# Kernel optimization log

Hardware: AMD Instinct MI355X
Metric: run time of the kernel (lower is better)

Reference implementation:

```python
import jax, jax.numpy as jnp
import numpy as np

B, T, C, H, N = 4, 1024, 1024, 16, 64
DW, DA, DV, DG = 64, 64, 64, 160  # LoRA ranks derived from C=1024
LNX_EPS = 0.00064


def layer_norm(h, g, b, eps=1e-5):
    m = h.mean(-1, keepdims=True)
    var = ((h - m) ** 2).mean(-1, keepdims=True)
    return (h - m) * jax.lax.rsqrt(var + eps) * g + b


def token_shift(h):
    # nn.ZeroPad2d((0,0,1,-1)): shift right along T, zero at t=0
    return jnp.pad(h, ((0, 0), (1, 0), (0, 0)))[:, :-1]


def wkv7(r, w, k, v, a, b):
    # RWKV-7 generalized recurrence. Inputs [B,T,C]; w is log-space decay.
    def re(t):
        return t.reshape(B, T, H, N).transpose(1, 0, 2, 3)  # -> [T,B,H,N]
    r, w, k, v, a, b = map(re, (r, w, k, v, a, b))
    dec = jnp.exp(-jnp.exp(w))
    S0 = jnp.zeros((B, H, N, N), r.dtype)  # state: [value_dim, key_dim]
    def step(S, ins):
        r_, d_, k_, v_, a_, b_ = ins
        sa = jnp.einsum('bhij,bhj->bhi', S, a_)
        S = S * d_[:, :, None, :] + sa[..., None] * b_[:, :, None, :] + v_[..., None] * k_[:, :, None, :]
        return S, jnp.einsum('bhij,bhj->bhi', S, r_)
    _, out = jax.lax.scan(step, S0, (r, dec, k, v, a, b))
    return out.transpose(1, 0, 2, 3).reshape(B, T, C)


def _forward(x, v_first, ln1_g, ln1_b, ln2_g, ln2_b, x_r, x_w, x_k_mix, x_v_mix, x_a, x_g,
             w0, w1, w2, a0, a1, a2, v0, v1, v2, g1, g2, k_k, k_a, r_k,
             W_r, W_k, W_v, W_o, lnx_g, lnx_b, xk_c, Wk_ff, Wv_ff):
    # ---- RNW_Tmix (original RWKV-7 path, layer_id > 0) ----
    h = layer_norm(x, ln1_g, ln1_b)
    xx = token_shift(h) - h
    xr = h + xx * x_r
    xw = h + xx * x_w
    xk = h + xx * x_k_mix
    xv = h + xx * x_v_mix
    xa = h + xx * x_a
    xg = h + xx * x_g
    r = xr @ W_r.T
    w = -jax.nn.softplus(-(w0 + jnp.tanh(xw @ w1) @ w2)) - 0.5
    k = xk @ W_k.T
    v = xv @ W_v.T
    v = v + (v_first - v) * jax.nn.sigmoid(v0 + (xv @ v1) @ v2)
    a = jax.nn.sigmoid(a0 + (xa @ a1) @ a2)
    g = jax.nn.sigmoid(xg @ g1) @ g2
    kk = (k * k_k).reshape(B, T, H, N)
    kk = kk / jnp.maximum(jnp.linalg.norm(kk, axis=-1, keepdims=True), 1e-12)
    kk = kk.reshape(B, T, C)
    k = k * (1 + (a - 1) * k_a)
    y = wkv7(r, w, k, v, -kk, kk * a)
    # GroupNorm(H groups of N channels), eps=0.00064
    yg = y.reshape(B, T, H, N)
    m = yg.mean(-1, keepdims=True)
    var = ((yg - m) ** 2).mean(-1, keepdims=True)
    y = ((yg - m) * jax.lax.rsqrt(var + LNX_EPS)).reshape(B, T, C) * lnx_g + lnx_b
    r4 = r.reshape(B, T, H, N)
    k4 = k.reshape(B, T, H, N)
    v4 = v.reshape(B, T, H, N)
    y = y + ((r4 * k4 * r_k).sum(-1, keepdims=True) * v4).reshape(B, T, C)
    x = x + (y * g) @ W_o.T
    # ---- RWKV_CMix_x070 ----
    h2 = layer_norm(x, ln2_g, ln2_b)
    hx = token_shift(h2) - h2
    kf = h2 + hx * xk_c
    kf = jnp.square(jax.nn.relu(kf @ Wk_ff.T))
    x = x + kf @ Wv_ff.T
    return x


def setup_inputs() -> dict:
    key = jax.random.key(0)
    ks = jax.random.split(key, 40)
    it = iter(range(40))
    def rn(shape, s=0.02):
        return (jax.random.normal(ks[next(it)], shape) * s).astype(jnp.float32)
    def ru(shape):
        return jax.random.uniform(ks[next(it)], shape).astype(jnp.float32)
    return {
        'x': rn((B, T, C), 1.0),
        'v_first': rn((B, T, C), 1.0),
        'ln1_g': jnp.ones((C,), jnp.float32), 'ln1_b': jnp.zeros((C,), jnp.float32),
        'ln2_g': jnp.ones((C,), jnp.float32), 'ln2_b': jnp.zeros((C,), jnp.float32),
        'x_r': ru((1, 1, C)), 'x_w': ru((1, 1, C)), 'x_k_mix': ru((1, 1, C)),
        'x_v_mix': ru((1, 1, C)), 'x_a': ru((1, 1, C)), 'x_g': ru((1, 1, C)),
        'w0': rn((1, 1, C), 0.5) - 4.0, 'w1': rn((C, DW)), 'w2': rn((DW, C), 0.1),
        'a0': rn((1, 1, C), 0.3), 'a1': rn((C, DA)), 'a2': rn((DA, C), 0.1),
        'v0': rn((1, 1, C), 0.3) + 0.73, 'v1': rn((C, DV)), 'v2': rn((DV, C), 0.1),
        'g1': rn((C, DG)), 'g2': rn((DG, C), 0.1),
        'k_k': rn((1, 1, C), 0.05) + 0.71, 'k_a': rn((1, 1, C), 0.05) + 1.02,
        'r_k': rn((H, N), 0.05) - 0.04,
        'W_r': rn((C, C)), 'W_k': rn((C, C), 0.002), 'W_v': rn((C, C)), 'W_o': rn((C, C)),
        'lnx_g': jnp.ones((C,), jnp.float32), 'lnx_b': jnp.zeros((C,), jnp.float32),
        'xk_c': ru((1, 1, C)),
        'Wk_ff': rn((4 * C, C)), 'Wv_ff': rn((C, 4 * C)),
    }


def reference(x, v_first, ln1_g, ln1_b, ln2_g, ln2_b, x_r, x_w, x_k_mix, x_v_mix, x_a, x_g,
              w0, w1, w2, a0, a1, a2, v0, v1, v2, g1, g2, k_k, k_a, r_k,
              W_r, W_k, W_v, W_o, lnx_g, lnx_b, xk_c, Wk_ff, Wv_ff):
    return _forward(x, v_first, ln1_g, ln1_b, ln2_g, ln2_b, x_r, x_w, x_k_mix, x_v_mix, x_a, x_g,
                    w0, w1, w2, a0, a1, a2, v0, v1, v2, g1, g2, k_k, k_a, r_k,
                    W_r, W_k, W_v, W_o, lnx_g, lnx_b, xk_c, Wk_ff, Wv_ff)
```

## Files before the change

kernel.cpp:

```cpp
#include <hip/hip_runtime.h>
#include <hip/hip_bf16.h>


#define BB 4
#define TT 1024
#define CC 1024
#define HH 16
#define NHEAD 64
#define MTOK 4096
#define FFDIM 4096

using bf16 = __hip_bfloat16;
typedef __attribute__((ext_vector_type(8))) short short8;
typedef __attribute__((ext_vector_type(4))) float f32x4;

__device__ __forceinline__ float b2f(bf16 x) { return __bfloat162float(x); }
__device__ __forceinline__ bf16 f2b(float x) { return __float2bfloat16(x); }
__device__ __forceinline__ float u2f(unsigned short u) {
  return __uint_as_float((unsigned)u << 16);
}
__device__ __forceinline__ float4 cv4(ushort4 u) {
  return make_float4(u2f(u.x), u2f(u.y), u2f(u.z), u2f(u.w));
}
__device__ __forceinline__ float ldin(const void* p, size_t i, int m) {
  return m ? b2f(((const bf16*)p)[i]) : ((const float*)p)[i];
}

__device__ __forceinline__ void async16(const void* g, void* l) {
  __builtin_amdgcn_global_load_lds((const __attribute__((address_space(1))) void*)g,
                                   (__attribute__((address_space(3))) void*)l, 16, 0, 0);
}

__device__ __forceinline__ float rowsum16(float x) {
  int t;
  t = __builtin_amdgcn_update_dpp(0, __float_as_int(x), 0x121, 0xF, 0xF, true);
  x += __int_as_float(t);
  t = __builtin_amdgcn_update_dpp(0, __float_as_int(x), 0x122, 0xF, 0xF, true);
  x += __int_as_float(t);
  t = __builtin_amdgcn_update_dpp(0, __float_as_int(x), 0x124, 0xF, 0xF, true);
  x += __int_as_float(t);
  t = __builtin_amdgcn_update_dpp(0, __float_as_int(x), 0x128, 0xF, 0xF, true);
  x += __int_as_float(t);
  return x;
}

__global__ void probe_kernel(const unsigned int* g, int* flag) {
  if (threadIdx.x == 0 && blockIdx.x == 0) {
    flag[0] = (g[0] == 0x3F800000u) ? 0 : 1;
    flag[1] = 1;
  }
}

__global__ __launch_bounds__(256) void cvt_all(
    const void* wr, const void* wk, const void* wv, const void* wo,
    const void* wkff, const void* wvff, const int* flagp,
    bf16* wrc, bf16* wkc, bf16* wvc, bf16* woc, bf16* wkffc, bf16* wvffc) {
  const int z = blockIdx.z;
  const void* in; bf16* out; int n4;
  const int nCC4 = CC * CC / 4, nFF4 = FFDIM * CC / 4;
  switch (z) {
    case 0: in = wr;   out = wrc;   n4 = nCC4; break;
    case 1: in = wk;   out = wkc;   n4 = nCC4; break;
    case 2: in = wv;   out = wvc;   n4 = nCC4; break;
    case 3: in = wo;   out = woc;   n4 = nCC4; break;
    case 4: in = wkff; out = wkffc; n4 = nFF4; break;
    default: in = wvff; out = wvffc; n4 = nFF4; break;
  }
  const int fl = *flagp;
  const int i4 = blockIdx.x * 256 + threadIdx.x;
  if (i4 >= n4) return;
  const size_t i = (size_t)i4 * 4;
#pragma unroll
  for (int e = 0; e < 4; ++e) out[i + e] = f2b(ldin(in, i + e, fl));
}

__global__ __launch_bounds__(256) void fillmark_kernel(unsigned short* out, int n) {
  const int i = blockIdx.x * 256 + threadIdx.x;
  if (i < n) out[i] = 0x3F80;
}

template<int XM>
__global__ __launch_bounds__(256) void ln_kernel(const void* __restrict__ x,
    const void* __restrict__ g, const void* __restrict__ be, const int* flagp,
    bf16* __restrict__ out, float eps) {
  const int fl = *flagp;
  const int xm = (XM < 0) ? fl : XM;
  const int tid = threadIdx.x;
  const size_t base = (size_t)blockIdx.x * CC + tid * 4;
  float v[4];
#pragma unroll
  for (int e = 0; e < 4; ++e) v[e] = ldin(x, base + e, xm);
  float s  = v[0] + v[1] + v[2] + v[3];
  float ss = v[0]*v[0] + v[1]*v[1] + v[2]*v[2] + v[3]*v[3];
#pragma unroll
  for (int m = 1; m <= 32; m <<= 1) { s += __shfl_xor(s, m); ss += __shfl_xor(ss, m); }
  __shared__ float red[8];
  const int wave = tid >> 6, lane = tid & 63;
  if (lane == 0) { red[wave] = s; red[4 + wave] = ss; }
  __syncthreads();
  s  = red[0] + red[1] + red[2] + red[3];
  ss = red[4] + red[5] + red[6] + red[7];
  const float mean = s * (1.0f / CC);
  const float var  = ss * (1.0f / CC) - mean * mean;
  const float rstd = rsqrtf(var + eps);
#pragma unroll
  for (int e = 0; e < 4; ++e) {
    const int c = tid * 4 + e;
    out[base + e] = f2b((v[e] - mean) * rstd * ldin(g, c, fl) + ldin(be, c, fl));
  }
}

__global__ __launch_bounds__(256) void mix6_kernel(const bf16* __restrict__ h,
    const void* cr, const void* cw, const void* ck,
    const void* cv, const void* ca, const void* cg, const int* flagp,
    bf16* __restrict__ xr, bf16* __restrict__ xw, bf16* __restrict__ xk,
    bf16* __restrict__ xv, bf16* __restrict__ xa, bf16* __restrict__ xg) {
  const int fl = *flagp;
  const size_t idx = (size_t)blockIdx.x * 256 + threadIdx.x;
  const int c = idx & (CC - 1);
  const int t = (idx >> 10) & (TT - 1);
  const float hv = b2f(h[idx]);
  const float xx = (t == 0 ? 0.f : b2f(h[idx - CC])) - hv;
  xr[idx] = f2b(hv + xx * ldin(cr, c, fl));
  xw[idx] = f2b(hv + xx * ldin(cw, c, fl));
  xk[idx] = f2b(hv + xx * ldin(ck, c, fl));
  xv[idx] = f2b(hv + xx * ldin(cv, c, fl));
  xa[idx] = f2b(hv + xx * ldin(ca, c, fl));
  xg[idx] = f2b(hv + xx * ldin(cg, c, fl));
}

__global__ __launch_bounds__(256) void mix1_kernel(const bf16* __restrict__ h,
    const void* cf, const int* flagp, bf16* __restrict__ out) {
  const int fl = *flagp;
  const size_t idx = (size_t)blockIdx.x * 256 + threadIdx.x;
  const int c = idx & (CC - 1);
  const int t = (idx >> 10) & (TT - 1);
  const float hv = b2f(h[idx]);
  const float xx = (t == 0 ? 0.f : b2f(h[idx - CC])) - hv;
  out[idx] = f2b(hv + xx * ldin(cf, c, fl));
}

__global__ __launch_bounds__(256) void transpose_all(
    const void* w1, const void* a1, const void* v1, const void* g1,
    const void* w2, const void* a2, const void* v2, const void* g2,
    const int* flagp,
    bf16* w1t, bf16* a1t, bf16* v1t, bf16* g1t,
    bf16* w2t, bf16* a2t, bf16* v2t, bf16* g2t) {
  const int z = blockIdx.z;
  const void* in; bf16* out; int R, Cc;
  switch (z) {
    case 0: in = w1; out = w1t; R = CC;  Cc = 64;  break;
    case 1: in = a1; out = a1t; R = CC;  Cc = 64;  break;
    case 2: in = v1; out = v1t; R = CC;  Cc = 64;  break;
    case 3: in = g1; out = g1t; R = CC;  Cc = 160; break;
    case 4: in = w2; out = w2t; R = 64;  Cc = CC;  break;
    case 5: in = a2; out = a2t; R = 64;  Cc = CC;  break;
    case 6: in = v2; out = v2t; R = 64;  Cc = CC;  break;
    default: in = g2; out = g2t; R = 160; Cc = CC; break;
  }
  const int fl = *flagp;
  const int idx = blockIdx.x * 256 + threadIdx.x;
  if (idx >= R * Cc) return;
  const int r = idx / Cc, c = idx - r * Cc;
  out[(size_t)c * R + r] = f2b(ldin(in, idx, fl));
}

__device__ __forceinline__ void gemm_core(const bf16* __restrict__ A,
    const bf16* __restrict__ Bm, bf16* __restrict__ Out, int M, int N, int K,
    int mode, short* As, short* Bs) {
  const int tid  = threadIdx.x;
  const int wave = tid >> 6;
  const int lane = tid & 63;
  const int m0 = blockIdx.y * 128;
  const int n0 = blockIdx.x * 128;
  const int wr = (wave >> 1) * 64;
  const int wc = (wave & 1) * 64;
  const int lrow = lane & 15;
  const int lq   = lane >> 4;
  f32x4 acc[4][4];
#pragma unroll
  for (int i = 0; i < 4; ++i)
#pragma unroll
    for (int j = 0; j < 4; ++j) acc[i][j] = (f32x4){0.f, 0.f, 0.f, 0.f};

  for (int k0 = 0; k0 < K; k0 += 32) {
#pragma unroll
    for (int j = 0; j < 2; ++j) {
      const int chunk = j * 256 + tid;
      const int row = chunk >> 2;
      const int c8  = (chunk & 3) * 8;
      const int ldsbase = (j * 256 + wave * 64) * 8;
      const bf16* ga = A + (size_t)(m0 + row) * K + (k0 + c8);
      int br = n0 + row; br = br < N ? br : N - 1;
      const bf16* gb = Bm + (size_t)br * K + (k0 + c8);
      async16(ga, &As[ldsbase]);
      async16(gb, &Bs[ldsbase]);
    }
    __syncthreads();
    short8 af[4], bfr[4];
#pragma unroll
    for (int mi = 0; mi < 4; ++mi)
      af[mi] = *(const short8*)&As[(wr + mi * 16 + lrow) * 32 + lq * 8];
#pragma unroll
    for (int ni = 0; ni < 4; ++ni)
      bfr[ni] = *(const short8*)&Bs[(wc + ni * 16 + lrow) * 32 + lq * 8];
#pragma unroll
    for (int mi = 0; mi < 4; ++mi)
#pragma unroll
      for (int ni = 0; ni < 4; ++ni)
        acc[mi][ni] = __builtin_amdgcn_mfma_f32_16x16x32_bf16(af[mi], bfr[ni], acc[mi][ni], 0, 0, 0);
    __syncthreads();
  }
#pragma unroll
  for (int mi = 0; mi < 4; ++mi) {
#pragma unroll
    for (int ni = 0; ni < 4; ++ni) {
      const int col = n0 + wc + ni * 16 + lrow;
      if (col < N) {
#pragma unroll
        for (int rr = 0; rr < 4; ++rr) {
          const int rowg = m0 + wr + mi * 16 + lq * 4 + rr;
          const size_t oidx = (size_t)rowg * N + col;
          const float val = acc[mi][ni][rr];
          if (mode == 1) { const float t = val > 0.f ? val : 0.f; Out[oidx] = f2b(t * t); }
          else if (mode == 2) Out[oidx] = f2b(val);
          else if (mode == 3) Out[oidx] = f2b(tanhf(val));
          else Out[oidx] = f2b(1.f / (1.f + expf(-val)));
        }
      }
    }
  }
}

template<int MODE>
__global__ __launch_bounds__(256) void gemm_mf(const bf16* __restrict__ A,
    const bf16* __restrict__ Bm, bf16* __restrict__ Out, int M, int N, int K) {
  __shared__ short As[128 * 32];
  __shared__ short Bs[128 * 32];
  gemm_core(A, Bm, Out, M, N, K, MODE, As, Bs);
}

__global__ __launch_bounds__(256) void gemm_lora1(
    const bf16* xw, const bf16* xa, const bf16* xv, const bf16* xg,
    const bf16* w1t, const bf16* a1t, const bf16* v1t, const bf16* g1t,
    bf16* wm, bf16* am, bf16* vm, bf16* gm) {
  __shared__ short As[128 * 32];
  __shared__ short Bs[128 * 32];
  const int z = blockIdx.z;
  const bf16* A; const bf16* B; bf16* O; int N; int mode;
  if (z == 0)      { A = xw; B = w1t; O = wm; N = 64;  mode = 3; }
  else if (z == 1) { A = xa; B = a1t; O = am; N = 64;  mode = 2; }
  else if (z == 2) { A = xv; B = v1t; O = vm; N = 64;  mode = 2; }
  else             { A = xg; B = g1t; O = gm; N = 160; mode = 4; }
  if ((int)blockIdx.x * 128 >= N) return;
  gemm_core(A, B, O, MTOK, N, CC, mode, As, Bs);
}

__global__ __launch_bounds__(256) void gemm_lora2(
    const bf16* wm, const bf16* am, const bf16* vm, const bf16* gm,
    const bf16* w2t, const bf16* a2t, const bf16* v2t, const bf16* g2t,
    bf16* wl, bf16* al, bf16* vl, bf16* gb) {
  __shared__ short As[128 * 32];
  __shared__ short Bs[128 * 32];
  const int z = blockIdx.z;
  const bf16* A; const bf16* B; bf16* O; int K;
  if (z == 0)      { A = wm; B = w2t; O = wl; K = 64;  }
  else if (z == 1) { A = am; B = a2t; O = al; K = 64;  }
  else if (z == 2) { A = vm; B = v2t; O = vl; K = 64;  }
  else             { A = gm; B = g2t; O = gb; K = 160; }
  gemm_core(A, B, O, MTOK, CC, K, 2, As, Bs);
}

template<int MODE>
__global__ __launch_bounds__(256) void gemm_bt(const bf16* __restrict__ A,
    const void* __restrict__ Bm, const int* bmp, bf16* __restrict__ Out,
    int M, int N, int K) {
  const int bm = *bmp;
  __shared__ float As[64][17];
  __shared__ float Bs[64][17];
  const int tid = threadIdx.x;
  const int m0 = blockIdx.y * 64;
  const int n0 = blockIdx.x * 64;
  const int ty = tid >> 4, tx = tid & 15;
  float acc[4][4] = {};
  for (int k0 = 0; k0 < K; k0 += 16) {
    __syncthreads();
#pragma unroll
    for (int e = 0; e < 4; ++e) {
      const int lin = e * 256 + tid;
      const int row = lin >> 4;
      const int kk  = lin & 15;
      As[row][kk] = b2f(A[(size_t)(m0 + row) * K + k0 + kk]);
      int br = n0 + row; br = br < N ? br : N - 1;
      Bs[row][kk] = ldin(Bm, (size_t)br * K + k0 + kk, bm);
    }
    __syncthreads();
#pragma unroll
    for (int k = 0; k < 16; ++k) {
      float a[4], b[4];
#pragma unroll
      for (int i = 0; i < 4; ++i) a[i] = As[ty * 4 + i][k];
#pragma unroll
      for (int j = 0; j < 4; ++j) b[j] = Bs[tx * 4 + j][k];
#pragma unroll
      for (int i = 0; i < 4; ++i)
#pragma unroll
        for (int j = 0; j < 4; ++j) acc[i][j] += a[i] * b[j];
    }
  }
#pragma unroll
  for (int i = 0; i < 4; ++i) {
    const int rowg = m0 + ty * 4 + i;
#pragma unroll
    for (int j = 0; j < 4; ++j) {
      const int col = n0 + tx * 4 + j;
      if (col < N) {
        const size_t oidx = (size_t)rowg * N + col;
        const float val = acc[i][j];
        if (MODE == 1) { const float t = val > 0.f ? val : 0.f; Out[oidx] = f2b(t * t); }
        else if (MODE == 2) Out[oidx] = f2b(val);
        else if (MODE == 3) Out[oidx] = f2b(tanhf(val));
        else Out[oidx] = f2b(1.f / (1.f + expf(-val)));
      }
    }
  }
}

__global__ __launch_bounds__(256) void combine_kernel(
    bf16* kf, bf16* vf, bf16* wl, bf16* al, bf16* vl,
    const void* vfirst, const void* w0, const void* a0, const void* v0,
    const void* kkp, const void* kap, const int* flagp, float* decp) {
  const int fl = *flagp;
  const int tid = threadIdx.x;
  const size_t base = (size_t)blockIdx.x * CC + tid * 4;
  float kkv[4], av4[4];
  float ssq = 0.f;
#pragma unroll
  for (int e = 0; e < 4; ++e) {
    const int c = tid * 4 + e;
    const size_t idx = base + e;
    const float u = ldin(w0, c, fl) + b2f(wl[idx]);
    const float w = (u > 0.f ? -log1pf(expf(-u)) : u - log1pf(expf(u))) - 0.5f;
    wl[idx] = f2b(w);
    if (decp) decp[idx] = __expf(-__expf(w));
    const float a  = 1.f / (1.f + expf(-(ldin(a0, c, fl) + b2f(al[idx]))));
    const float vg = 1.f / (1.f + expf(-(ldin(v0, c, fl) + b2f(vl[idx]))));
    const float v = b2f(vf[idx]);
    vf[idx] = f2b(v + (ldin(vfirst, idx, fl) - v) * vg);
    const float kv = b2f(kf[idx]);
    const float kkr = kv * ldin(kkp, c, fl);
    kkv[e] = kkr; av4[e] = a;
    ssq += kkr * kkr;
    kf[idx] = f2b(kv * (1.f + (a - 1.f) * ldin(kap, c, fl)));
  }
  ssq += __shfl_xor(ssq, 1); ssq += __shfl_xor(ssq, 2);
  ssq += __shfl_xor(ssq, 4); ssq += __shfl_xor(ssq, 8);
  const float inv = 1.f / fmaxf(sqrtf(ssq), 1e-12f);
#pragma unroll
  for (int e = 0; e < 4; ++e) {
    const size_t idx = base + e;
    const float kkn = kkv[e] * inv;
    al[idx] = f2b(-kkn);
    vl[idx] = f2b(kkn * av4[e]);
  }
}


template<int DF>
__device__ __forceinline__ void wkv_stage(const bf16* rp, const void* wp,
    const bf16* kp, const bf16* vp, const bf16* ap, const bf16* bp,
    size_t cb, char* sb, int wave, int lane) {
  const int hb = wave & 1;
  const size_t g2 = cb + (size_t)(hb * 8 + (lane >> 3)) * CC + (lane & 7) * 8;
  if (wave < 2) {
    async16(rp + g2, sb + 0    + hb * 1024);
    async16(kp + g2, sb + 2048 + hb * 1024);
    async16(ap + g2, sb + 4096 + hb * 1024);
  } else {
    async16(bp + g2, sb + 6144 + hb * 1024);
    async16(vp + g2, sb + 8192 + hb * 1024);
  }
  if constexpr (DF) {
    const size_t gd = cb + (size_t)(wave * 4 + (lane >> 4)) * CC + (lane & 15) * 4;
    async16((const float*)wp + gd, sb + 10240 + wave * 1024);
  } else {
    if (wave >= 2) async16((const bf16*)wp + g2, sb + 10240 + hb * 1024);
  }
}

template<int DF>
__device__ __forceinline__ void wkv_load_step(const char* sb, int t, int j0, int i,
    float4& rv, float4& dv, float4& av, float4& bv, float4& vk) {
  const short* sR = (const short*)sb;
  const short* sK = (const short*)(sb + 2048);
  const short* sA = (const short*)(sb + 4096);
  const short* sB = (const short*)(sb + 6144);
  const unsigned short* sV = (const unsigned short*)(sb + 8192);
  rv = cv4(*(const ushort4*)(const void*)(sR + t * 64 + j0));
  const float4 kv = cv4(*(const ushort4*)(const void*)(sK + t * 64 + j0));
  av = cv4(*(const ushort4*)(const void*)(sA + t * 64 + j0));
  bv = cv4(*(const ushort4*)(const void*)(sB + t * 64 + j0));
  const float vi = u2f(sV[t * 64 + i]);
  if constexpr (DF) {
    const float* sD = (const float*)(sb + 10240);
    dv = *(const float4*)(const void*)(sD + t * 64 + j0);
  } else {
    const short* sW = (const short*)(sb + 10240);
    const float4 wv = cv4(*(const ushort4*)(const void*)(sW + t * 64 + j0));
    dv = make_float4(__expf(-__expf(wv.x)), __expf(-__expf(wv.y)),
                     __expf(-__expf(wv.z)), __expf(-__expf(wv.w)));
  }
  vk = make_float4(vi * kv.x, vi * kv.y, vi * kv.z, vi * kv.w);
}

template<int DF>
__global__ __launch_bounds__(256) void wkv_scan(
    const bf16* __restrict__ rp, const void* __restrict__ wp,
    const bf16* __restrict__ kp, const bf16* __restrict__ vp,
    const bf16* __restrict__ ap, const bf16* __restrict__ bp,
    bf16* __restrict__ yp) {
  constexpr int BUFB = DF ? 14336 : 12288;
  __shared__ char sbuf[2][BUFB];
  const int blk = blockIdx.x;
  const int q = blk & 3;
  const int h = (blk >> 2) & (HH - 1);
  const int b = blk >> 6;
  const int tid = threadIdx.x;
  const int wave = tid >> 6;
  const int lane = tid & 63;
  const int rl = tid >> 4;
  const int jq = tid & 15;
  const int j0 = jq * 4;
  const int i = q * 16 + rl;
  const size_t bbase = (size_t)b * TT * CC + (size_t)h * NHEAD;

  float4 S = make_float4(0.f, 0.f, 0.f, 0.f);

  wkv_stage<DF>(rp, wp, kp, vp, ap, bp, bbase, sbuf[0], wave, lane);
  __syncthreads();

  for (int c = 0; c < TT / 16; ++c) {
    if (c + 1 < TT / 16)
      wkv_stage<DF>(rp, wp, kp, vp, ap, bp, bbase + (size_t)(c + 1) * 16 * CC,
                    sbuf[(c + 1) & 1], wave, lane);
    const char* sb = sbuf[c & 1];
    size_t yb = bbase + (size_t)c * 16 * CC + i;

    float4 rv, dv, av, bv, vk;
    wkv_load_step<DF>(sb, 0, j0, i, rv, dv, av, bv, vk);
#pragma unroll
    for (int s = 0; s < 16; ++s) {
      float4 rv2, dv2, av2, bv2, vk2;
      if (s + 1 < 16)
        wkv_load_step<DF>(sb, s + 1, j0, i, rv2, dv2, av2, bv2, vk2);
      float p0 = S.x * av.x + S.y * av.y;
      float p1 = S.z * av.z + S.w * av.w;
      const float sa = rowsum16(p0 + p1);
      S.x = fmaf(S.x, dv.x, fmaf(sa, bv.x, vk.x));
      S.y = fmaf(S.y, dv.y, fmaf(sa, bv.y, vk.y));
      S.z = fmaf(S.z, dv.z, fmaf(sa, bv.z, vk.z));
      S.w = fmaf(S.w, dv.w, fmaf(sa, bv.w, vk.w));
      float q0 = S.x * rv.x + S.y * rv.y;
      float q1 = S.z * rv.z + S.w * rv.w;
      const float o = rowsum16(q0 + q1);
      if (jq == 0) yp[yb] = f2b(o);
      yb += CC;
      if (s + 1 < 16) { rv = rv2; dv = dv2; av = av2; bv = bv2; vk = vk2; }
    }
    __syncthreads();
  }
}

__global__ __launch_bounds__(256) void post_kernel(
    const bf16* __restrict__ y, const bf16* __restrict__ rp, const bf16* __restrict__ kp,
    const bf16* __restrict__ vp, const bf16* __restrict__ gp,
    const void* rk, const void* lnxg, const void* lnxb, const int* flagp,
    bf16* __restrict__ out) {
  const int fl = *flagp;
  const int tid = threadIdx.x;
  const size_t base = (size_t)blockIdx.x * CC + tid * 4;
  float yv[4];
  float s = 0.f, ssq = 0.f, dot = 0.f;
#pragma unroll
  for (int e = 0; e < 4; ++e) {
    const size_t idx = base + e;
    yv[e] = b2f(y[idx]);
    s += yv[e]; ssq += yv[e] * yv[e];
    dot += b2f(rp[idx]) * b2f(kp[idx]) * ldin(rk, tid * 4 + e, fl);
  }
  s   += __shfl_xor(s, 1);   s   += __shfl_xor(s, 2);   s   += __shfl_xor(s, 4);   s   += __shfl_xor(s, 8);
  ssq += __shfl_xor(ssq, 1); ssq += __shfl_xor(ssq, 2); ssq += __shfl_xor(ssq, 4); ssq += __shfl_xor(ssq, 8);
  dot += __shfl_xor(dot, 1); dot += __shfl_xor(dot, 2); dot += __shfl_xor(dot, 4); dot += __shfl_xor(dot, 8);
  const float m = s * (1.f / NHEAD);
  const float var = ssq * (1.f / NHEAD) - m * m;
  const float rs = rsqrtf(var + 0.00064f);
#pragma unroll
  for (int e = 0; e < 4; ++e) {
    const int c = tid * 4 + e;
    const size_t idx = base + e;
    const float yo = (yv[e] - m) * rs * ldin(lnxg, c, fl) + ldin(lnxb, c, fl)
                     + dot * b2f(vp[idx]);
    out[idx] = f2b(yo * b2f(gp[idx]));
  }
}

__global__ __launch_bounds__(256) void addres_kernel(const void* x, const int* flagp,
    const bf16* __restrict__ o, float* __restrict__ out) {
  const int fl = *flagp;
  const size_t idx = (size_t)blockIdx.x * 256 + threadIdx.x;
  out[idx] = ldin(x, idx, fl) + b2f(o[idx]);
}

__global__ __launch_bounds__(256) void final_kernel(const float* __restrict__ x1,
    const bf16* __restrict__ f, const int* flagp, void* out) {
  const int fl = *flagp;
  const size_t idx = (size_t)blockIdx.x * 256 + threadIdx.x;
  const float v = x1[idx] + b2f(f[idx]);
  if (fl) ((bf16*)out)[idx] = f2b(v);
  else    ((float*)out)[idx] = v;
}

extern "C" void kernel_launch(void* const* d_in, const int* in_sizes, int n_in,
                              void* d_out, int out_size, void* d_ws, size_t ws_size,
                              hipStream_t stream) {
  const void* X      = d_in[0];
  const void* VFIRST = d_in[1];
  const void* LN1G = d_in[2];
  const void* LN1B = d_in[3];
  const void* LN2G = d_in[4];
  const void* LN2B = d_in[5];
  const void* XRC = d_in[6];
  const void* XWC = d_in[7];
  const void* XKC = d_in[8];
  const void* XVC = d_in[9];
  const void* XAC = d_in[10];
  const void* XGC = d_in[11];
  const void* W0p = d_in[12];
  const void* W1p = d_in[13];
  const void* W2p = d_in[14];
  const void* A0p = d_in[15];
  const void* A1p = d_in[16];
  const void* A2p = d_in[17];
  const void* V0p = d_in[18];
  const void* V1p = d_in[19];
  const void* V2p = d_in[20];
  const void* G1p = d_in[21];
  const void* G2p = d_in[22];
  const void* KKp = d_in[23];
  const void* KAp = d_in[24];
  const void* RKp = d_in[25];
  const void* WR  = d_in[26];
  const void* WK  = d_in[27];
  const void* WV  = d_in[28];
  const void* WO  = d_in[29];
  const void* LNXG = d_in[30];
  const void* LNXB = d_in[31];
  const void* XKCF = d_in[32];
  const void* WKFF = d_in[33];
  const void* WVFF = d_in[34];

  const size_t BTC  = (size_t)MTOK * CC;
  const size_t SLOT = BTC * 2;
  char* ws = (char*)d_ws;

  size_t off = 8 * SLOT;
  auto alloc = [&](size_t n) { size_t o = off; off += (n + 255) & ~(size_t)255; return o; };
  const size_t oW1T = alloc((size_t)CC * 64 * 2);
  const size_t oA1T = alloc((size_t)CC * 64 * 2);
  const size_t oV1T = alloc((size_t)CC * 64 * 2);
  const size_t oG1T = alloc((size_t)CC * 160 * 2);
  const size_t oW2T = alloc((size_t)CC * 64 * 2);
  const size_t oA2T = alloc((size_t)CC * 64 * 2);
  const size_t oV2T = alloc((size_t)CC * 64 * 2);
  const size_t oG2T = alloc((size_t)CC * 160 * 2);
  const size_t oWM  = alloc((size_t)MTOK * 64 * 2);
  const size_t oAM  = alloc((size_t)MTOK * 64 * 2);
  const size_t oVM  = alloc((size_t)MTOK * 64 * 2);
  const size_t oGM  = alloc((size_t)MTOK * 160 * 2);
  const size_t oFLG = alloc(8);
  const size_t baseNeed = off;
  const size_t oDEC = alloc(BTC * 4);
  const size_t decNeed = off;
  const size_t oWRc   = alloc((size_t)CC * CC * 2);
  const size_t oWKc   = alloc((size_t)CC * CC * 2);
  const size_t oWVc   = alloc((size_t)CC * CC * 2);
  const size_t oWOc   = alloc((size_t)CC * CC * 2);
  const size_t oWKFFc = alloc((size_t)FFDIM * CC * 2);
  const size_t oWVFFc = alloc((size_t)CC * FFDIM * 2);
  const size_t mfmaNeed = off;

  if (baseNeed > ws_size) {
    fillmark_kernel<<<(out_size + 255) / 256, 256, 0, stream>>>(
        (unsigned short*)d_out, out_size);
    return;
  }
  const bool hasdec = (decNeed <= ws_size);
  const bool useMF  = (mfmaNeed <= ws_size);

  int* FLAG = (int*)(ws + oFLG);
  int* ONE  = FLAG + 1;

  bf16* B0 = (bf16*)(ws + 0 * SLOT);
  bf16* B1 = (bf16*)(ws + 1 * SLOT);
  bf16* B2 = (bf16*)(ws + 2 * SLOT);
  bf16* B3 = (bf16*)(ws + 3 * SLOT);
  bf16* B4 = (bf16*)(ws + 4 * SLOT);
  bf16* B5 = (bf16*)(ws + 5 * SLOT);
  bf16* B6 = (bf16*)(ws + 6 * SLOT);
  bf16* B7 = (bf16*)(ws + 7 * SLOT);
  bf16* Hb  = B0;
  bf16* XRb = B1; bf16* XWb = B2; bf16* XKb = B3;
  bf16* XVb = B4; bf16* XAb = B5; bf16* XGb = B6;
  bf16* Rb  = B7;
  bf16* Kg  = B0;
  bf16* Vg  = B1;
  bf16* WLb = B2;
  bf16* ALb = B3;
  bf16* VLb = B4;
  bf16* Gb  = B5;
  bf16* Yb  = B6;
  bf16* YG  = B2;
  bf16* OBb = B0;
  float* X1b = (float*)(ws + 2 * SLOT);
  bf16* H2b  = B1;
  bf16* KFIN = B0;
  bf16* KACT = B4;
  bf16* FFNb = B1;

  bf16* W1T = (bf16*)(ws + oW1T);
  bf16* A1T = (bf16*)(ws + oA1T);
  bf16* V1T = (bf16*)(ws + oV1T);
  bf16* G1T = (bf16*)(ws + oG1T);
  bf16* W2T = (bf16*)(ws + oW2T);
  bf16* A2T = (bf16*)(ws + oA2T);
  bf16* V2T = (bf16*)(ws + oV2T);
  bf16* G2T = (bf16*)(ws + oG2T);
  bf16* WM  = (bf16*)(ws + oWM);
  bf16* AM  = (bf16*)(ws + oAM);
  bf16* VM  = (bf16*)(ws + oVM);
  bf16* GM  = (bf16*)(ws + oGM);
  float* DECb = (float*)(ws + oDEC);
  float* DECarg = hasdec ? DECb : (float*)nullptr;
  bf16* WRc   = (bf16*)(ws + oWRc);
  bf16* WKc   = (bf16*)(ws + oWKc);
  bf16* WVc   = (bf16*)(ws + oWVc);
  bf16* WOc   = (bf16*)(ws + oWOc);
  bf16* WKFFc = (bf16*)(ws + oWKFFc);
  bf16* WVFFc = (bf16*)(ws + oWVFFc);

  const int EW = (int)(BTC / 256);
  const dim3 blk256(256);

  probe_kernel<<<1, 1, 0, stream>>>((const unsigned int*)LN1G, FLAG);

  ln_kernel<-1><<<MTOK, blk256, 0, stream>>>(X, LN1G, LN1B, FLAG, Hb, 1e-5f);
  mix6_kernel<<<EW, blk256, 0, stream>>>(Hb, XRC, XWC, XKC, XVC, XAC, XGC, FLAG,
                                         XRb, XWb, XKb, XVb, XAb, XGb);
  transpose_all<<<dim3(640, 1, 8), blk256, 0, stream>>>(
      W1p, A1p, V1p, G1p, W2p, A2p, V2p, G2p, FLAG,
      W1T, A1T, V1T, G1T, W2T, A2T, V2T, G2T);

  if (useMF) {
    cvt_all<<<dim3(4096, 1, 6), blk256, 0, stream>>>(
        WR, WK, WV, WO, WKFF, WVFF, FLAG, WRc, WKc, WVc, WOc, WKFFc, WVFFc);

    const dim3 gCC(8, 32), gFF1(32, 32);
    gemm_lora1<<<dim3(2, 32, 4), blk256, 0, stream>>>(
        XWb, XAb, XVb, XGb, W1T, A1T, V1T, G1T, WM, AM, VM, GM);
    gemm_mf<2><<<gCC, blk256, 0, stream>>>(XRb, WRc, Rb, MTOK, CC, CC);
    gemm_mf<2><<<gCC, blk256, 0, stream>>>(XKb, WKc, Kg, MTOK, CC, CC);
    gemm_mf<2><<<gCC, blk256, 0, stream>>>(XVb, WVc, Vg, MTOK, CC, CC);
    gemm_lora2<<<dim3(8, 32, 4), blk256, 0, stream>>>(
        WM, AM, VM, GM, W2T, A2T, V2T, G2T, WLb, ALb, VLb, Gb);

    combine_kernel<<<MTOK, blk256, 0, stream>>>(Kg, Vg, WLb, ALb, VLb, VFIRST,
                                                W0p, A0p, V0p, KKp, KAp, FLAG, DECarg);
    if (hasdec)
      wkv_scan<1><<<BB * HH * 4, blk256, 0, stream>>>(Rb, DECb, Kg, Vg, ALb, VLb, Yb);
    else
      wkv_scan<0><<<BB * HH * 4, blk256, 0, stream>>>(Rb, WLb, Kg, Vg, ALb, VLb, Yb);
    post_kernel<<<MTOK, blk256, 0, stream>>>(Yb, Rb, Kg, Vg, Gb, RKp, LNXG, LNXB, FLAG, YG);
    gemm_mf<2><<<gCC, blk256, 0, stream>>>(YG, WOc, OBb, MTOK, CC, CC);
    addres_kernel<<<EW, blk256, 0, stream>>>(X, FLAG, OBb, X1b);

    ln_kernel<0><<<MTOK, blk256, 0, stream>>>(X1b, LN2G, LN2B, FLAG, H2b, 1e-5f);
    mix1_kernel<<<EW, blk256, 0, stream>>>(H2b, XKCF, FLAG, KFIN);
    gemm_mf<1><<<gFF1, blk256, 0, stream>>>(KFIN, WKFFc, KACT, MTOK, FFDIM, CC);
    gemm_mf<2><<<gCC, blk256, 0, stream>>>(KACT, WVFFc, FFNb, MTOK, CC, FFDIM);
    final_kernel<<<EW, blk256, 0, stream>>>(X1b, FFNb, FLAG, d_out);
  } else {
    const dim3 gCC(16, 64), gL1(1, 64), gG1(3, 64), gFF1(64, 64);
    gemm_bt<3><<<gL1, blk256, 0, stream>>>(XWb, W1T, ONE, WM, MTOK, 64, CC);
    gemm_bt<2><<<gL1, blk256, 0, stream>>>(XAb, A1T, ONE, AM, MTOK, 64, CC);
    gemm_bt<2><<<gL1, blk256, 0, stream>>>(XVb, V1T, ONE, VM, MTOK, 64, CC);
    gemm_bt<4><<<gG1, blk256, 0, stream>>>(XGb, G1T, ONE, GM, MTOK, 160, CC);
    gemm_bt<2><<<gCC, blk256, 0, stream>>>(XRb, WR, FLAG, Rb, MTOK, CC, CC);
    gemm_bt<2><<<gCC, blk256, 0, stream>>>(XKb, WK, FLAG, Kg, MTOK, CC, CC);
    gemm_bt<2><<<gCC, blk256, 0, stream>>>(XVb, WV, FLAG, Vg, MTOK, CC, CC);
    gemm_bt<2><<<gCC, blk256, 0, stream>>>(WM, W2T, ONE, WLb, MTOK, CC, 64);
    gemm_bt<2><<<gCC, blk256, 0, stream>>>(AM, A2T, ONE, ALb, MTOK, CC, 64);
    gemm_bt<2><<<gCC, blk256, 0, stream>>>(VM, V2T, ONE, VLb, MTOK, CC, 64);
    gemm_bt<2><<<gCC, blk256, 0, stream>>>(GM, G2T, ONE, Gb, MTOK, CC, 160);

    combine_kernel<<<MTOK, blk256, 0, stream>>>(Kg, Vg, WLb, ALb, VLb, VFIRST,
                                                W0p, A0p, V0p, KKp, KAp, FLAG, DECarg);
    if (hasdec)
      wkv_scan<1><<<BB * HH * 4, blk256, 0, stream>>>(Rb, DECb, Kg, Vg, ALb, VLb, Yb);
    else
      wkv_scan<0><<<BB * HH * 4, blk256, 0, stream>>>(Rb, WLb, Kg, Vg, ALb, VLb, Yb);
    post_kernel<<<MTOK, blk256, 0, stream>>>(Yb, Rb, Kg, Vg, Gb, RKp, LNXG, LNXB, FLAG, YG);
    gemm_bt<2><<<gCC, blk256, 0, stream>>>(YG, WO, FLAG, OBb, MTOK, CC, CC);
    addres_kernel<<<EW, blk256, 0, stream>>>(X, FLAG, OBb, X1b);

    ln_kernel<0><<<MTOK, blk256, 0, stream>>>(X1b, LN2G, LN2B, FLAG, H2b, 1e-5f);
    mix1_kernel<<<EW, blk256, 0, stream>>>(H2b, XKCF, FLAG, KFIN);
    gemm_bt<1><<<gFF1, blk256, 0, stream>>>(KFIN, WKFF, FLAG, KACT, MTOK, FFDIM, CC);
    gemm_bt<2><<<gCC, blk256, 0, stream>>>(KACT, WVFF, FLAG, FFNb, MTOK, CC, FFDIM);
    final_kernel<<<EW, blk256, 0, stream>>>(X1b, FFNb, FLAG, d_out);
  }

  (void)in_sizes; (void)n_in; (void)out_size;
}
```

Before: 824.7 us.

## Split WKV scan over 8 blocks per head with two state columns per thread

The WKV recurrence kernel now launches 8 blocks per (batch, head) instead of 4. Each thread holds 2 state elements instead of 4, and each row's reduction spans 32 lanes, using an extra ds_swizzle step after the DPP row sum. This doubles parallelism on the serial scan, which previously used only 256 blocks, to shorten the critical path per time step. In exchange it duplicates the staging of r/k/a/b/w loads across twice as many blocks and adds one cross-row swizzle per reduction.

```diff
diff --git a/kernel.cpp b/kernel.cpp
--- a/kernel.cpp
+++ b/kernel.cpp
@@ -19,8 +19,8 @@
 __device__ __forceinline__ float u2f(unsigned short u) {
   return __uint_as_float((unsigned)u << 16);
 }
-__device__ __forceinline__ float4 cv4(ushort4 u) {
-  return make_float4(u2f(u.x), u2f(u.y), u2f(u.z), u2f(u.w));
+__device__ __forceinline__ float2 cv2(ushort2 u) {
+  return make_float2(u2f(u.x), u2f(u.y));
 }
 __device__ __forceinline__ float ldin(const void* p, size_t i, int m) {
   return m ? b2f(((const bf16*)p)[i]) : ((const float*)p)[i];
@@ -41,6 +41,12 @@
   x += __int_as_float(t);
   t = __builtin_amdgcn_update_dpp(0, __float_as_int(x), 0x128, 0xF, 0xF, true);
   x += __int_as_float(t);
+  return x;
+}
+
+__device__ __forceinline__ float rowsum32(float x) {
+  x = rowsum16(x);
+  x += __int_as_float(__builtin_amdgcn_ds_swizzle(__float_as_int(x), 0x401F));
   return x;
 }
 
@@ -390,27 +396,26 @@
 
 template<int DF>
 __device__ __forceinline__ void wkv_load_step(const char* sb, int t, int j0, int i,
-    float4& rv, float4& dv, float4& av, float4& bv, float4& vk) {
+    float2& rv, float2& dv, float2& av, float2& bv, float2& vk) {
   const short* sR = (const short*)sb;
   const short* sK = (const short*)(sb + 2048);
   const short* sA = (const short*)(sb + 4096);
   const short* sB = (const short*)(sb + 6144);
   const unsigned short* sV = (const unsigned short*)(sb + 8192);
-  rv = cv4(*(const ushort4*)(const void*)(sR + t * 64 + j0));
-  const float4 kv = cv4(*(const ushort4*)(const void*)(sK + t * 64 + j0));
-  av = cv4(*(const ushort4*)(const void*)(sA + t * 64 + j0));
-  bv = cv4(*(const ushort4*)(const void*)(sB + t * 64 + j0));
+  rv = cv2(*(const ushort2*)(const void*)(sR + t * 64 + j0));
+  const float2 kv = cv2(*(const ushort2*)(const void*)(sK + t * 64 + j0));
+  av = cv2(*(const ushort2*)(const void*)(sA + t * 64 + j0));
+  bv = cv2(*(const ushort2*)(const void*)(sB + t * 64 + j0));
   const float vi = u2f(sV[t * 64 + i]);
   if constexpr (DF) {
     const float* sD = (const float*)(sb + 10240);
-    dv = *(const float4*)(const void*)(sD + t * 64 + j0);
+    dv = *(const float2*)(const void*)(sD + t * 64 + j0);
   } else {
     const short* sW = (const short*)(sb + 10240);
-    const float4 wv = cv4(*(const ushort4*)(const void*)(sW + t * 64 + j0));
-    dv = make_float4(__expf(-__expf(wv.x)), __expf(-__expf(wv.y)),
-                     __expf(-__expf(wv.z)), __expf(-__expf(wv.w)));
-  }
-  vk = make_float4(vi * kv.x, vi * kv.y, vi * kv.z, vi * kv.w);
+    const float2 wv = cv2(*(const ushort2*)(const void*)(sW + t * 64 + j0));
+    dv = make_float2(__expf(-__expf(wv.x)), __expf(-__expf(wv.y)));
+  }
+  vk = make_float2(vi * kv.x, vi * kv.y);
 }
 
 template<int DF>
@@ -422,19 +427,19 @@
   constexpr int BUFB = DF ? 14336 : 12288;
   __shared__ char sbuf[2][BUFB];
   const int blk = blockIdx.x;
-  const int q = blk & 3;
-  const int h = (blk >> 2) & (HH - 1);
-  const int b = blk >> 6;
+  const int q = blk & 7;
+  const int h = (blk >> 3) & (HH - 1);
+  const int b = blk >> 7;
   const int tid = threadIdx.x;
   const int wave = tid >> 6;
   const int lane = tid & 63;
-  const int rl = tid >> 4;
-  const int jq = tid & 15;
-  const int j0 = jq * 4;
-  const int i = q * 16 + rl;
+  const int rl = tid >> 5;
+  const int jq = tid & 31;
+  const int j0 = jq * 2;
+  const int i = q * 8 + rl;
   const size_t bbase = (size_t)b * TT * CC + (size_t)h * NHEAD;
 
-  float4 S = make_float4(0.f, 0.f, 0.f, 0.f);
+  float2 S = make_float2(0.f, 0.f);
 
   wkv_stage<DF>(rp, wp, kp, vp, ap, bp, bbase, sbuf[0], wave, lane);
   __syncthreads();
@@ -446,23 +451,19 @@
     const char* sb = sbuf[c & 1];
     size_t yb = bbase + (size_t)c * 16 * CC + i;
 
-    float4 rv, dv, av, bv, vk;
+    float2 rv, dv, av, bv, vk;
     wkv_load_step<DF>(sb, 0, j0, i, rv, dv, av, bv, vk);
 #pragma unroll
     for (int s = 0; s < 16; ++s) {
-      float4 rv2, dv2, av2, bv2, vk2;
+      float2 rv2, dv2, av2, bv2, vk2;
       if (s + 1 < 16)
         wkv_load_step<DF>(sb, s + 1, j0, i, rv2, dv2, av2, bv2, vk2);
-      float p0 = S.x * av.x + S.y * av.y;
-      float p1 = S.z * av.z + S.w * av.w;
-      const float sa = rowsum16(p0 + p1);
+      const float p = fmaf(S.y, av.y, S.x * av.x);
+      const float sa = rowsum32(p);
       S.x = fmaf(S.x, dv.x, fmaf(sa, bv.x, vk.x));
       S.y = fmaf(S.y, dv.y, fmaf(sa, bv.y, vk.y));
-      S.z = fmaf(S.z, dv.z, fmaf(sa, bv.z, vk.z));
-      S.w = fmaf(S.w, dv.w, fmaf(sa, bv.w, vk.w));
-      float q0 = S.x * rv.x + S.y * rv.y;
-      float q1 = S.z * rv.z + S.w * rv.w;
-      const float o = rowsum16(q0 + q1);
+      const float qv = fmaf(S.y, rv.y, S.x * rv.x);
+      const float o = rowsum32(qv);
       if (jq == 0) yp[yb] = f2b(o);
       yb += CC;
       if (s + 1 < 16) { rv = rv2; dv = dv2; av = av2; bv = bv2; vk = vk2; }
@@ -676,9 +677,9 @@
     combine_kernel<<<MTOK, blk256, 0, stream>>>(Kg, Vg, WLb, ALb, VLb, VFIRST,
                                                 W0p, A0p, V0p, KKp, KAp, FLAG, DECarg);
     if (hasdec)
-      wkv_scan<1><<<BB * HH * 4, blk256, 0, stream>>>(Rb, DECb, Kg, Vg, ALb, VLb, Yb);
+      wkv_scan<1><<<BB * HH * 8, blk256, 0, stream>>>(Rb, DECb, Kg, Vg, ALb, VLb, Yb);
     else
-      wkv_scan<0><<<BB * HH * 4, blk256, 0, stream>>>(Rb, WLb, Kg, Vg, ALb, VLb, Yb);
+      wkv_scan<0><<<BB * HH * 8, blk256, 0, stream>>>(Rb, WLb, Kg, Vg, ALb, VLb, Yb);
     post_kernel<<<MTOK, blk256, 0, stream>>>(Yb, Rb, Kg, Vg, Gb, RKp, LNXG, LNXB, FLAG, YG);
     gemm_mf<2><<<gCC, blk256, 0, stream>>>(YG, WOc, OBb, MTOK, CC, CC);
     addres_kernel<<<EW, blk256, 0, stream>>>(X, FLAG, OBb, X1b);
@@ -705,9 +706,9 @@
     combine_kernel<<<MTOK, blk256, 0, stream>>>(Kg, Vg, WLb, ALb, VLb, VFIRST,
                                                 W0p, A0p, V0p, KKp, KAp, FLAG, DECarg);
     if (hasdec)
-      wkv_scan<1><<<BB * HH * 4, blk256, 0, stream>>>(Rb, DECb, Kg, Vg, ALb, VLb, Yb);
+      wkv_scan<1><<<BB * HH * 8, blk256, 0, stream>>>(Rb, DECb, Kg, Vg, ALb, VLb, Yb);
     else
-      wkv_scan<0><<<BB * HH * 4, blk256, 0, stream>>>(Rb, WLb, Kg, Vg, ALb, VLb, Yb);
+      wkv_scan<0><<<BB * HH * 8, blk256, 0, stream>>>(Rb, WLb, Kg, Vg, ALb, VLb, Yb);
     post_kernel<<<MTOK, blk256, 0, stream>>>(Yb, Rb, Kg, Vg, Gb, RKp, LNXG, LNXB, FLAG, YG);
     gemm_bt<2><<<gCC, blk256, 0, stream>>>(YG, WO, FLAG, OBb, MTOK, CC, CC);
     addres_kernel<<<EW, blk256, 0, stream>>>(X, FLAG, OBb, X1b);
```

Result: slower. 851.5 us (+3.2%).
